# Performance work log

Measured on AMD Instinct MI355X. Metric: run time of the kernel, lower is better.

## Reference

```python
import jax, jax.numpy as jnp
import numpy as np

# Dims: B batch, L seq, D model dim, A attn dim, H heads, W window, FF ff hidden
B, L, D = 4, 4096, 1024
A, H, W = 64, 1, 64
FF = 2 * D
EPS = 1e-6


def setup_inputs() -> dict:
    key = jax.random.key(0)
    ks = jax.random.split(key, 12)
    s = lambda k, shape, scale: (jax.random.normal(k, shape, jnp.float32) * scale)
    return {
        "x": s(ks[0], (B, L, D), 1.0),
        "norm1_w": jnp.ones((D,), jnp.float32),
        "norm2_w": jnp.ones((D,), jnp.float32),
        "a_raw": s(ks[1], (D,), 1.0),   # diag SSM transition (pre-sigmoid)
        "b_w": s(ks[2], (D,), 0.5),     # diag input gain
        "c_w": s(ks[3], (D,), 0.5),     # diag output gain
        "Wq": s(ks[4], (D, A), D ** -0.5),
        "Wk": s(ks[5], (D, A), D ** -0.5),
        "Wv": s(ks[6], (D, A), D ** -0.5),
        "Wo": s(ks[7], (A, D), A ** -0.5),
        "Wg": s(ks[8], (D, 1), D ** -0.5),
        "gate_bias": jnp.float32(-4.0),
        "ff_w1": s(ks[9], (D, FF), D ** -0.5),
        "ff_w2": s(ks[10], (FF, D), FF ** -0.5),
    }


def rmsnorm(x, w):
    return x * jax.lax.rsqrt(jnp.mean(x * x, -1, keepdims=True) + EPS) * w


def ssm_scan(u, a):
    # h_t = a * h_{t-1} + u_t (diagonal linear recurrence), parallel assoc scan over time
    aa = jnp.broadcast_to(a, u.shape)

    def comb(c1, c2):
        a1, b1 = c1
        a2, b2 = c2
        return a1 * a2, a2 * b1 + b2

    _, h = jax.lax.associative_scan(comb, (aa, u), axis=1)
    return h


def reference(x, norm1_w, norm2_w, a_raw, b_w, c_w, Wq, Wk, Wv, Wo, Wg, gate_bias, ff_w1, ff_w2):
    normed = rmsnorm(x, norm1_w)                      # input_norm
    a = jax.nn.sigmoid(a_raw)                         # decay in (0,1)
    h = ssm_scan(normed * b_w, a)                     # ChaosSSMCore diag scan
    x_ssm = x + h * c_w                               # residual

    # Causal sliding-window attention sidecar (window W, includes self)
    K = x_ssm @ Wk                                    # [B,L,A]
    V = x_ssm @ Wv
    hd = A // H
    q = (x_ssm @ Wq).reshape(B, L, H, hd)
    idx = jnp.arange(L)[:, None] + jnp.arange(W)[None, :] - (W - 1)  # [L,W]
    valid = idx >= 0
    idxc = jnp.clip(idx, 0, L - 1)
    Kg = K[:, idxc].reshape(B, L, W, H, hd)           # gathered window keys
    Vg = V[:, idxc].reshape(B, L, W, H, hd)
    scores = jnp.einsum('blhd,blwhd->blhw', q, Kg) / jnp.sqrt(jnp.float32(hd))
    scores = jnp.where(valid[None, :, None, :], scores, -jnp.inf)
    p = jax.nn.softmax(scores, axis=-1)
    attn = jnp.einsum('blhw,blwhd->blhd', p, Vg).reshape(B, L, A) @ Wo

    gate = jax.nn.sigmoid(x_ssm @ Wg + gate_bias)     # near-zero gate at init
    x_ssm = x_ssm + gate * attn

    n2 = rmsnorm(x_ssm, norm2_w)                      # ff_norm
    y = x_ssm + jax.nn.silu(n2 @ ff_w1) @ ff_w2       # FeedForward residual
    return y
```

## Files before the change

### kernel.cpp

```cpp
#include <hip/hip_runtime.h>
#include <math.h>

#define B_ 4
#define L_ 4096
#define D_ 1024
#define A_ 64
#define FF_ 2048
#define N_ (B_*L_)
#define EPS_ 1e-6f
#define CHUNK_ 128
#define NCHUNK_ (L_/CHUNK_)

typedef __attribute__((ext_vector_type(8))) short bf16x8;
typedef __attribute__((ext_vector_type(4))) short s16x4;
typedef __attribute__((ext_vector_type(4))) float f32x4;

static __device__ __forceinline__ float sigmoidf_(float x) { return 1.f/(1.f+expf(-x)); }
static __device__ __forceinline__ float siluf_(float x)    { return x/(1.f+expf(-x)); }

static __device__ __forceinline__ unsigned short f2bf(float f) {
    unsigned u = __float_as_uint(f);
    u += 0x7fffu + ((u >> 16) & 1u);
    return (unsigned short)(u >> 16);
}

static __device__ __forceinline__ void gload16(const short* g, short* l) {
    __builtin_amdgcn_global_load_lds(
        (const __attribute__((address_space(1))) void*)g,
        (__attribute__((address_space(3))) void*)l, 16, 0, 0);
}

__global__ __launch_bounds__(256) void rms_kernel(const float* __restrict__ x,
                                                  float* __restrict__ rms)
{
    int row  = blockIdx.x*4 + (threadIdx.x>>6);
    int lane = threadIdx.x & 63;
    const float4* xr = (const float4*)(x + (size_t)row*D_);
    float s = 0.f;
#pragma unroll
    for (int j = 0; j < 4; j++) {
        float4 v = xr[lane + 64*j];
        s += v.x*v.x + v.y*v.y + v.z*v.z + v.w*v.w;
    }
#pragma unroll
    for (int off = 32; off > 0; off >>= 1) s += __shfl_xor(s, off);
    if (lane == 0) rms[row] = rsqrtf(s*(1.f/(float)D_) + EPS_);
}

__global__ __launch_bounds__(64) void scan1_kernel(
    const float* __restrict__ x, const float* __restrict__ rms1,
    const float* __restrict__ n1w, const float* __restrict__ bw,
    const float* __restrict__ araw, float* __restrict__ cpart)
{
    int d = blockIdx.x*64 + threadIdx.x;
    int c = blockIdx.y;
    int b = blockIdx.z;
    float a = sigmoidf_(araw[d]);
    float w = n1w[d]*bw[d];
    float h = 0.f;
    size_t base = ((size_t)b*L_ + (size_t)c*CHUNK_)*D_ + d;
    const float* rp = rms1 + b*L_ + c*CHUNK_;
#pragma unroll 8
    for (int t = 0; t < CHUNK_; t++) {
        float u = x[base + (size_t)t*D_] * rp[t] * w;
        h = a*h + u;
    }
    cpart[((size_t)b*NCHUNK_ + c)*D_ + d] = h;
}

__global__ __launch_bounds__(256) void scan2_kernel(
    const float* __restrict__ araw, const float* __restrict__ cpart,
    float* __restrict__ cin)
{
    int idx = blockIdx.x*256 + threadIdx.x;
    int b = idx >> 10;
    int d = idx & (D_-1);
    float a = sigmoidf_(araw[d]);
    float aT = a;
#pragma unroll
    for (int i = 0; i < 7; i++) aT *= aT;
    float cy = 0.f;
    for (int c = 0; c < NCHUNK_; c++) {
        size_t o = ((size_t)b*NCHUNK_ + c)*D_ + d;
        cin[o] = cy;
        cy = aT*cy + cpart[o];
    }
}

__global__ __launch_bounds__(64) void scan3_kernel(
    const float* __restrict__ x, const float* __restrict__ rms1,
    const float* __restrict__ n1w, const float* __restrict__ bw,
    const float* __restrict__ cw, const float* __restrict__ araw,
    const float* __restrict__ cin, float* __restrict__ x_ssm,
    short* __restrict__ xsb)
{
    int d = blockIdx.x*64 + threadIdx.x;
    int c = blockIdx.y;
    int b = blockIdx.z;
    float a = sigmoidf_(araw[d]);
    float w = n1w[d]*bw[d];
    float cwd = cw[d];
    float h = cin[((size_t)b*NCHUNK_ + c)*D_ + d];
    size_t base = ((size_t)b*L_ + (size_t)c*CHUNK_)*D_ + d;
    const float* rp = rms1 + b*L_ + c*CHUNK_;
#pragma unroll 8
    for (int t = 0; t < CHUNK_; t++) {
        size_t p = base + (size_t)t*D_;
        float xv = x[p];
        h = a*h + xv * rp[t] * w;
        float o = xv + h*cwd;
        x_ssm[p] = o;
        xsb[p] = (short)f2bf(o);
    }
}

__global__ __launch_bounds__(256) void gate_kernel(
    const float* __restrict__ xs, const float* __restrict__ Wg,
    const float* __restrict__ gb, float* __restrict__ gate)
{
    int row  = blockIdx.x*4 + (threadIdx.x>>6);
    int lane = threadIdx.x & 63;
    const float4* xr = (const float4*)(xs + (size_t)row*D_);
    const float4* wr = (const float4*)Wg;
    float s = 0.f;
#pragma unroll
    for (int j = 0; j < 4; j++) {
        float4 xv = xr[lane + 64*j];
        float4 wv = wr[lane + 64*j];
        s += xv.x*wv.x + xv.y*wv.y + xv.z*wv.z + xv.w*wv.w;
    }
#pragma unroll
    for (int off = 32; off > 0; off >>= 1) s += __shfl_xor(s, off);
    if (lane == 0) gate[row] = sigmoidf_(s + gb[0]);
}

__global__ __launch_bounds__(256) void attn_kernel(
    const float* __restrict__ qm, const float* __restrict__ km,
    const float* __restrict__ vm, short* __restrict__ om)
{
    __shared__ float KV[128][68];
    int b  = blockIdx.y;
    int l0 = blockIdx.x*64;
    int t  = threadIdx.x;
    int r  = t >> 2;
    int qq = t & 3;

#pragma unroll
    for (int i = 0; i < 8; i++) {
        int lin = i*256 + t;
        int row = lin >> 4;
        int f4  = lin & 15;
        int gl  = l0 - 64 + row;
        float4 val = make_float4(0.f,0.f,0.f,0.f);
        if (gl >= 0) val = *(const float4*)(km + ((size_t)b*L_ + gl)*A_ + f4*4);
        *(float4*)&KV[row][f4*4] = val;
    }
    float4 qreg[16];
    {
        const float* qrow = qm + ((size_t)b*L_ + l0 + r)*A_;
#pragma unroll
        for (int j = 0; j < 16; j++) qreg[j] = *(const float4*)(qrow + j*4);
    }
    __syncthreads();

    float s[16];
#pragma unroll
    for (int wi = 0; wi < 16; wi++) {
        int w  = qq*16 + wi;
        int tr = r + w + 1;
        float dot = 0.f;
#pragma unroll
        for (int j = 0; j < 16; j++) {
            float4 kv = *(const float4*)&KV[tr][j*4];
            dot += qreg[j].x*kv.x + qreg[j].y*kv.y + qreg[j].z*kv.z + qreg[j].w*kv.w;
        }
        s[wi] = (l0 + r - 63 + w >= 0) ? dot*0.125f : -INFINITY;
    }
    float mx = s[0];
#pragma unroll
    for (int wi = 1; wi < 16; wi++) mx = fmaxf(mx, s[wi]);
    mx = fmaxf(mx, __shfl_xor(mx, 1));
    mx = fmaxf(mx, __shfl_xor(mx, 2));
    float sum = 0.f;
#pragma unroll
    for (int wi = 0; wi < 16; wi++) { s[wi] = expf(s[wi] - mx); sum += s[wi]; }
    sum += __shfl_xor(sum, 1);
    sum += __shfl_xor(sum, 2);
    float inv = 1.f/sum;
#pragma unroll
    for (int wi = 0; wi < 16; wi++) s[wi] *= inv;

    __syncthreads();
#pragma unroll
    for (int i = 0; i < 8; i++) {
        int lin = i*256 + t;
        int row = lin >> 4;
        int f4  = lin & 15;
        int gl  = l0 - 64 + row;
        float4 val = make_float4(0.f,0.f,0.f,0.f);
        if (gl >= 0) val = *(const float4*)(vm + ((size_t)b*L_ + gl)*A_ + f4*4);
        *(float4*)&KV[row][f4*4] = val;
    }
    __syncthreads();

    float4 acc[4];
#pragma unroll
    for (int ss = 0; ss < 4; ss++) acc[ss] = make_float4(0.f,0.f,0.f,0.f);
#pragma unroll
    for (int w = 0; w < 64; w++) {
        float pv = __shfl(s[w & 15], (t & 60) + (w >> 4));
        int tr = r + w + 1;
#pragma unroll
        for (int ss = 0; ss < 4; ss++) {
            float4 vv = *(const float4*)&KV[tr][qq*16 + ss*4];
            acc[ss].x += pv*vv.x; acc[ss].y += pv*vv.y;
            acc[ss].z += pv*vv.z; acc[ss].w += pv*vv.w;
        }
    }
    short* orow = om + ((size_t)b*L_ + l0 + r)*A_ + qq*16;
#pragma unroll
    for (int ss = 0; ss < 4; ss++) {
        s16x4 ov = { (short)f2bf(acc[ss].x), (short)f2bf(acc[ss].y),
                     (short)f2bf(acc[ss].z), (short)f2bf(acc[ss].w) };
        *(s16x4*)(orow + ss*4) = ov;
    }
}

__global__ __launch_bounds__(256) void cvt_transpose(
    const float* __restrict__ in, int R, int C, short* __restrict__ out)
{
    __shared__ short sh[64][68];
    int t  = threadIdx.x;
    int c0 = blockIdx.x * 64, r0 = blockIdx.y * 64;
    int rr = t >> 4, cc = (t & 15) * 4;
#pragma unroll
    for (int p = 0; p < 4; p++) {
        int r = p*16 + rr;
        float4 v = *(const float4*)(in + (size_t)(r0 + r)*C + c0 + cc);
        s16x4 sv = { (short)f2bf(v.x), (short)f2bf(v.y), (short)f2bf(v.z), (short)f2bf(v.w) };
        *(s16x4*)&sh[r][cc] = sv;
    }
    __syncthreads();
#pragma unroll
    for (int p = 0; p < 4; p++) {
        int c = p*16 + rr;
        s16x4 ov = { sh[cc+0][c], sh[cc+1][c], sh[cc+2][c], sh[cc+3][c] };
        *(s16x4*)(out + (size_t)(c0 + c)*R + r0 + cc) = ov;
    }
}

__global__ __launch_bounds__(256) void ff1prep(
    const float* __restrict__ xatt, const float* __restrict__ n2w,
    short* __restrict__ a1)
{
    int row  = blockIdx.x*4 + (threadIdx.x>>6);
    int lane = threadIdx.x & 63;
    const float4* xr = (const float4*)(xatt + (size_t)row*D_);
    const float4* wr = (const float4*)n2w;
    float4 v[4];
    float s = 0.f;
#pragma unroll
    for (int j = 0; j < 4; j++) {
        v[j] = xr[lane + 64*j];
        s += v[j].x*v[j].x + v[j].y*v[j].y + v[j].z*v[j].z + v[j].w*v[j].w;
    }
#pragma unroll
    for (int off = 32; off > 0; off >>= 1) s += __shfl_xor(s, off);
    float r = rsqrtf(s*(1.f/(float)D_) + EPS_);
#pragma unroll
    for (int j = 0; j < 4; j++) {
        float4 w = wr[lane + 64*j];
        s16x4 o = { (short)f2bf(v[j].x*r*w.x), (short)f2bf(v[j].y*r*w.y),
                    (short)f2bf(v[j].z*r*w.z), (short)f2bf(v[j].w*r*w.w) };
        *(s16x4*)(a1 + (size_t)row*D_ + (lane + 64*j)*4) = o;
    }
}

__global__ __launch_bounds__(256) void qkv_mfma(
    const short* __restrict__ A, const short* __restrict__ BT,
    float* __restrict__ qo, float* __restrict__ ko, float* __restrict__ vo)
{
    __shared__ short As2[2][64*32];
    __shared__ short Bs2[2][192*32];
    const int t = threadIdx.x, l = t & 63, w = t >> 6;
    const size_t m0 = (size_t)blockIdx.x*64;
    const short* Ab = A + m0*D_;

    const int ar = w*16 + (l&15);
    const int offA = ar*32 + (((l>>4) ^ ((ar>>1)&3)) & 3)*8;
    int offB[12];
#pragma unroll
    for (int j = 0; j < 12; j++) {
        int br = j*16 + (l&15);
        offB[j] = br*32 + (((l>>4) ^ ((br>>1)&3)) & 3)*8;
    }

#define QSTG(bi, k0) { \
        { int r = t>>2; int lc = (t&3) ^ ((r>>1)&3); \
          gload16(Ab + (size_t)r*D_ + (k0) + lc*8, &As2[bi][(w*64)*8]); } \
        _Pragma("unroll") \
        for (int i_ = 0; i_ < 3; i_++) { \
            int s_ = i_*256 + t; int r = s_>>2; int lc = (s_&3) ^ ((r>>1)&3); \
            gload16(BT + (size_t)r*D_ + (k0) + lc*8, &Bs2[bi][(i_*256 + w*64)*8]); } }

    f32x4 acc[12];
    f32x4 zero = {0.f,0.f,0.f,0.f};
#pragma unroll
    for (int j = 0; j < 12; j++) acc[j] = zero;

    QSTG(0, 0);
    __syncthreads();
    int cur = 0;
    for (int kt = 0; kt < 32; kt++) {
        if (kt + 1 < 32) QSTG(cur^1, (kt+1)*32);
        bf16x8 af = *(const bf16x8*)&As2[cur][offA];
#pragma unroll
        for (int j = 0; j < 12; j++) {
            bf16x8 bfv = *(const bf16x8*)&Bs2[cur][offB[j]];
            acc[j] = __builtin_amdgcn_mfma_f32_16x16x32_bf16(af, bfv, acc[j], 0, 0, 0);
        }
        __syncthreads();
        cur ^= 1;
    }
#pragma unroll
    for (int j = 0; j < 12; j++) {
        int col = j*16 + (l&15);
        int mat = col >> 6, c = col & 63;
        float* dst = (mat == 0) ? qo : (mat == 1) ? ko : vo;
#pragma unroll
        for (int v = 0; v < 4; v++) {
            size_t row = m0 + w*16 + (l>>4)*4 + v;
            dst[row*A_ + c] = acc[j][v];
        }
    }
#undef QSTG
}

__global__ __launch_bounds__(256) void gemm_wo(
    const short* __restrict__ A,
    const short* __restrict__ BT,
    const float* __restrict__ gate, const float* __restrict__ resid,
    float* __restrict__ Cout)
{
    __shared__ short As3[128*64];
    __shared__ short Bs3[128*64];
    const int t = threadIdx.x, l = t & 63, w = t >> 6;
    const int wm = w >> 1, wn = w & 1;
    const size_t m0 = (size_t)blockIdx.x*128, n0 = (size_t)blockIdx.y*128;

#pragma unroll
    for (int i = 0; i < 4; i++) {
        int s = i*256 + t;
        int r = s >> 3, lc = (s&7) ^ (r&7);
        gload16(A  + (m0 + r)*64 + lc*8, &As3[(i*256 + w*64)*8]);
        gload16(BT + (n0 + r)*64 + lc*8, &Bs3[(i*256 + w*64)*8]);
    }
    __syncthreads();

    f32x4 acc[4][4];
    f32x4 zero = {0.f,0.f,0.f,0.f};
#pragma unroll
    for (int i = 0; i < 4; i++)
#pragma unroll
        for (int j = 0; j < 4; j++) acc[i][j] = zero;

#pragma unroll
    for (int kk = 0; kk < 2; kk++) {
        bf16x8 af[4], bfv[4];
#pragma unroll
        for (int i = 0; i < 4; i++) {
            int ar = wm*64 + i*16 + (l&15);
            int pch = (kk*4 + (l>>4)) ^ (ar&7);
            af[i] = *(const bf16x8*)&As3[ar*64 + pch*8];
        }
#pragma unroll
        for (int j = 0; j < 4; j++) {
            int br = wn*64 + j*16 + (l&15);
            int pch = (kk*4 + (l>>4)) ^ (br&7);
            bfv[j] = *(const bf16x8*)&Bs3[br*64 + pch*8];
        }
#pragma unroll
        for (int i = 0; i < 4; i++)
#pragma unroll
            for (int j = 0; j < 4; j++)
                acc[i][j] = __builtin_amdgcn_mfma_f32_16x16x32_bf16(af[i], bfv[j], acc[i][j], 0, 0, 0);
    }

#pragma unroll
    for (int i = 0; i < 4; i++) {
#pragma unroll
        for (int v = 0; v < 4; v++) {
            size_t row = m0 + wm*64 + i*16 + (l>>4)*4 + v;
            float g = gate[row];
#pragma unroll
            for (int j = 0; j < 4; j++) {
                size_t col = n0 + wn*64 + j*16 + (l&15);
                Cout[row*D_ + col] = resid[row*D_ + col] + g*acc[i][j][v];
            }
        }
    }
}

template<int K, int MODE>
__global__ __launch_bounds__(512, 2) void gemm256(
    const short* __restrict__ A,
    const short* __restrict__ BT,
    void* __restrict__ Cout, int ldc)
{
    __shared__ short As[4][256*32];
    __shared__ short Bs[4][256*32];

    const int gy = gridDim.y;
    const int nwg = gridDim.x * gy;
    const int o = blockIdx.y * gridDim.x + blockIdx.x;
    const int q = nwg >> 3;
    const int swz = (o & 7)*q + (o >> 3);
    const int bx = swz / gy, by = swz % gy;

    const int t = threadIdx.x;
    const int l = t & 63;
    const int w = t >> 6;
    const int wm = w >> 2;
    const int wn = w & 3;
    const size_t m0 = (size_t)bx * 256;
    const size_t n0 = (size_t)by * 256;
    const short* Ab = A  + m0 * (size_t)K;
    const short* Bb = BT + n0 * (size_t)K;
    const int s0 = w*64 + l;

    int offA[8], offB[4];
#pragma unroll
    for (int i = 0; i < 8; i++) {
        int ar = wm*128 + i*16 + (l&15);
        offA[i] = ar*32 + (((l>>4) ^ ((ar>>1)&3)) & 3)*8;
    }
#pragma unroll
    for (int j = 0; j < 4; j++) {
        int br = wn*64 + j*16 + (l&15);
        offB[j] = br*32 + (((l>>4) ^ ((br>>1)&3)) & 3)*8;
    }

#define STAGE_A(bi, k0) { _Pragma("unroll") \
    for (int i_ = 0; i_ < 2; i_++) { \
        int s_ = i_*512 + s0; int r_ = s_>>2; int lc_ = (s_&3) ^ ((r_>>1)&3); \
        gload16(Ab + (size_t)r_*K + (k0) + lc_*8, &As[bi][(i_*512 + w*64)*8]); } }
#define STAGE_B(bi, k0) { _Pragma("unroll") \
    for (int i_ = 0; i_ < 2; i_++) { \
        int s_ = i_*512 + s0; int r_ = s_>>2; int lc_ = (s_&3) ^ ((r_>>1)&3); \
        gload16(Bb + (size_t)r_*K + (k0) + lc_*8, &Bs[bi][(i_*512 + w*64)*8]); } }

    f32x4 acc[8][4];
    f32x4 zero = {0.f,0.f,0.f,0.f};
#pragma unroll
    for (int i = 0; i < 8; i++)
#pragma unroll
        for (int j = 0; j < 4; j++) acc[i][j] = zero;

    STAGE_A(0, 0);  STAGE_B(0, 0);
    STAGE_A(1, 32); STAGE_B(1, 32);
    asm volatile("s_waitcnt vmcnt(4)" ::: "memory");
    __builtin_amdgcn_s_barrier();

    const int nk = K >> 5;
#pragma unroll 1
    for (int kt = 0; kt < nk; kt++) {
        const short* a_ = &As[kt & 3][0];
        const short* b_ = &Bs[kt & 3][0];
        const int prefetch = (kt + 2 < nk);
        const int pb = (kt + 2) & 3;
        const int pk = (kt + 2) << 5;

        bf16x8 bfv[4], af[4];
#pragma unroll
        for (int j = 0; j < 4; j++) bfv[j] = *(const bf16x8*)(b_ + offB[j]);
#pragma unroll
        for (int i = 0; i < 4; i++) af[i] = *(const bf16x8*)(a_ + offA[i]);
        if (prefetch) STAGE_A(pb, pk);
        __builtin_amdgcn_s_setprio(1);
#pragma unroll
        for (int i = 0; i < 4; i++)
#pragma unroll
            for (int j = 0; j < 4; j++)
                acc[i][j] = __builtin_amdgcn_mfma_f32_16x16x32_bf16(af[i], bfv[j], acc[i][j], 0, 0, 0);
        __builtin_amdgcn_s_setprio(0);

#pragma unroll
        for (int i = 0; i < 4; i++) af[i] = *(const bf16x8*)(a_ + offA[4+i]);
        if (prefetch) STAGE_B(pb, pk);
        __builtin_amdgcn_s_setprio(1);
#pragma unroll
        for (int i = 0; i < 4; i++)
#pragma unroll
            for (int j = 0; j < 4; j++)
                acc[4+i][j] = __builtin_amdgcn_mfma_f32_16x16x32_bf16(af[i], bfv[j], acc[4+i][j], 0, 0, 0);
        __builtin_amdgcn_s_setprio(0);

        if (prefetch) { asm volatile("s_waitcnt vmcnt(4)" ::: "memory"); }
        else          { asm volatile("s_waitcnt vmcnt(0)" ::: "memory"); }
        __builtin_amdgcn_s_barrier();
    }

#pragma unroll
    for (int i = 0; i < 8; i++) {
        size_t row_base = m0 + wm*128 + i*16 + (l >> 4)*4;
#pragma unroll
        for (int j = 0; j < 4; j++) {
            size_t col = n0 + wn*64 + j*16 + (l & 15);
#pragma unroll
            for (int v = 0; v < 4; v++) {
                size_t row = row_base + v;
                float val = acc[i][j][v];
                if (MODE == 0) {
                    ((short*)Cout)[row * ldc + col] = (short)f2bf(siluf_(val));
                } else {
                    float* p = (float*)Cout + row * ldc + col;
                    *p = val + *p;
                }
            }
        }
    }
#undef STAGE_A
#undef STAGE_B
}

extern "C" void kernel_launch(void* const* d_in, const int* in_sizes, int n_in,
                              void* d_out, int out_size, void* d_ws, size_t ws_size,
                              hipStream_t stream)
{
    const float* x    = (const float*)d_in[0];
    const float* n1w  = (const float*)d_in[1];
    const float* n2w  = (const float*)d_in[2];
    const float* araw = (const float*)d_in[3];
    const float* bw   = (const float*)d_in[4];
    const float* cw   = (const float*)d_in[5];
    const float* Wq   = (const float*)d_in[6];
    const float* Wk   = (const float*)d_in[7];
    const float* Wv   = (const float*)d_in[8];
    const float* Wo   = (const float*)d_in[9];
    const float* Wg   = (const float*)d_in[10];
    const float* gb   = (const float*)d_in[11];
    const float* ffw1 = (const float*)d_in[12];
    const float* ffw2 = (const float*)d_in[13];
    float* out = (float*)d_out;

    float* ws    = (float*)d_ws;
    float* rms1  = ws;
    float* gate  = rms1  + N_;
    float* cpart = gate  + N_;
    float* cin   = cpart + (size_t)B_*NCHUNK_*D_;
    float* qb    = cin   + (size_t)B_*NCHUNK_*D_;
    float* kb    = qb    + (size_t)N_*A_;
    float* vb    = kb    + (size_t)N_*A_;
    float* x_ssm = vb    + (size_t)N_*A_;
    short* xsb   = (short*)(x_ssm + (size_t)N_*D_);
    short* attnb = xsb   + (size_t)N_*D_;
    short* a1    = attnb + (size_t)N_*A_;
    short* act   = a1    + (size_t)N_*D_;
    short* w1t   = act   + (size_t)N_*FF_;
    short* w2t   = w1t   + (size_t)FF_*D_;
    short* wqkvT = w2t   + (size_t)D_*FF_;
    short* wot   = wqkvT + (size_t)192*D_;

    cvt_transpose<<<dim3(FF_/64, D_/64), 256, 0, stream>>>(ffw1, D_, FF_, w1t);
    cvt_transpose<<<dim3(D_/64, FF_/64), 256, 0, stream>>>(ffw2, FF_, D_, w2t);
    cvt_transpose<<<dim3(1, D_/64), 256, 0, stream>>>(Wq, D_, A_, wqkvT);
    cvt_transpose<<<dim3(1, D_/64), 256, 0, stream>>>(Wk, D_, A_, wqkvT + (size_t)A_*D_);
    cvt_transpose<<<dim3(1, D_/64), 256, 0, stream>>>(Wv, D_, A_, wqkvT + (size_t)2*A_*D_);
    cvt_transpose<<<dim3(D_/64, 1), 256, 0, stream>>>(Wo, A_, D_, wot);

    rms_kernel<<<N_/4, 256, 0, stream>>>(x, rms1);
    scan1_kernel<<<dim3(D_/64, NCHUNK_, B_), 64, 0, stream>>>(x, rms1, n1w, bw, araw, cpart);
    scan2_kernel<<<(B_*D_)/256, 256, 0, stream>>>(araw, cpart, cin);
    scan3_kernel<<<dim3(D_/64, NCHUNK_, B_), 64, 0, stream>>>(x, rms1, n1w, bw, cw, araw, cin, x_ssm, xsb);
    qkv_mfma<<<N_/64, 256, 0, stream>>>(xsb, wqkvT, qb, kb, vb);
    gate_kernel<<<N_/4, 256, 0, stream>>>(x_ssm, Wg, gb, gate);
    attn_kernel<<<dim3(L_/64, B_), 256, 0, stream>>>(qb, kb, vb, attnb);
    gemm_wo<<<dim3(N_/128, D_/128), 256, 0, stream>>>(attnb, wot, gate, x_ssm, out);
    ff1prep<<<N_/4, 256, 0, stream>>>(out, n2w, a1);
    gemm256<D_, 0><<<dim3(N_/256, FF_/256), 512, 0, stream>>>(a1, w1t, (void*)act, FF_);
    gemm256<FF_, 1><<<dim3(N_/256, D_/256), 512, 0, stream>>>(act, w2t, (void*)out, D_);
}
```

Before: 478.2 us.

## Rewrite FFN GEMMs as 8-phase ping-pong pipeline and merge QKV weight transposes

The FFN GEMM kernel is restructured to use K-tiles of 64, double-buffered half-tiles of A and B in a single 128KB LDS array with XOR swizzle, and four MFMA phases per iteration. Each phase is separated by barriers that interleave global-to-LDS prefetch of the next tile with compute, in the style of the public 8-wave ping-pong schedule. The warp-to-tile mapping also changes to a 2x4 interleaved layout. Separately, the three Q/K/V weight transposes are merged into one launch. The deeper schedule adds more barriers and uses LDS that could limit occupancy to 2 blocks per CU.

Result: slower. 494.6 us (+3.4%).

```diff
diff --git a/kernel.cpp b/kernel.cpp
--- a/kernel.cpp
+++ b/kernel.cpp
@@ -249,6 +249,32 @@
     }
 }
 
+__global__ __launch_bounds__(256) void qkv_t3(
+    const float* __restrict__ Wq, const float* __restrict__ Wk,
+    const float* __restrict__ Wv, short* __restrict__ outall)
+{
+    __shared__ short sh[64][68];
+    const float* in = (blockIdx.z == 0) ? Wq : (blockIdx.z == 1) ? Wk : Wv;
+    short* out = outall + (size_t)blockIdx.z * A_ * D_;
+    int t  = threadIdx.x;
+    int r0 = blockIdx.y * 64;
+    int rr = t >> 4, cc = (t & 15) * 4;
+#pragma unroll
+    for (int p = 0; p < 4; p++) {
+        int r = p*16 + rr;
+        float4 v = *(const float4*)(in + (size_t)(r0 + r)*A_ + cc);
+        s16x4 sv = { (short)f2bf(v.x), (short)f2bf(v.y), (short)f2bf(v.z), (short)f2bf(v.w) };
+        *(s16x4*)&sh[r][cc] = sv;
+    }
+    __syncthreads();
+#pragma unroll
+    for (int p = 0; p < 4; p++) {
+        int c = p*16 + rr;
+        s16x4 ov = { sh[cc+0][c], sh[cc+1][c], sh[cc+2][c], sh[cc+3][c] };
+        *(s16x4*)(out + (size_t)c*D_ + r0 + cc) = ov;
+    }
+}
+
 __global__ __launch_bounds__(256) void ff1prep(
     const float* __restrict__ xatt, const float* __restrict__ n2w,
     short* __restrict__ a1)
@@ -402,52 +428,55 @@
 }
 
 template<int K, int MODE>
-__global__ __launch_bounds__(512, 2) void gemm256(
+__global__ __launch_bounds__(512, 2) void gemm8p(
     const short* __restrict__ A,
     const short* __restrict__ BT,
     void* __restrict__ Cout, int ldc)
 {
-    __shared__ short As[4][256*32];
-    __shared__ short Bs[4][256*32];
-
-    const int gy = gridDim.y;
-    const int nwg = gridDim.x * gy;
-    const int o = blockIdx.y * gridDim.x + blockIdx.x;
+    __shared__ short LDSb[65536];
+
+    const int gx = gridDim.x, gy = gridDim.y;
+    const int nwg = gx*gy;
+    const int o = blockIdx.y*gx + blockIdx.x;
     const int q = nwg >> 3;
     const int swz = (o & 7)*q + (o >> 3);
     const int bx = swz / gy, by = swz % gy;
 
-    const int t = threadIdx.x;
-    const int l = t & 63;
-    const int w = t >> 6;
-    const int wm = w >> 2;
-    const int wn = w & 3;
-    const size_t m0 = (size_t)bx * 256;
-    const size_t n0 = (size_t)by * 256;
-    const short* Ab = A  + m0 * (size_t)K;
-    const short* Bb = BT + n0 * (size_t)K;
-    const int s0 = w*64 + l;
-
-    int offA[8], offB[4];
-#pragma unroll
-    for (int i = 0; i < 8; i++) {
-        int ar = wm*128 + i*16 + (l&15);
-        offA[i] = ar*32 + (((l>>4) ^ ((ar>>1)&3)) & 3)*8;
-    }
-#pragma unroll
-    for (int j = 0; j < 4; j++) {
-        int br = wn*64 + j*16 + (l&15);
-        offB[j] = br*32 + (((l>>4) ^ ((br>>1)&3)) & 3)*8;
-    }
-
-#define STAGE_A(bi, k0) { _Pragma("unroll") \
-    for (int i_ = 0; i_ < 2; i_++) { \
-        int s_ = i_*512 + s0; int r_ = s_>>2; int lc_ = (s_&3) ^ ((r_>>1)&3); \
-        gload16(Ab + (size_t)r_*K + (k0) + lc_*8, &As[bi][(i_*512 + w*64)*8]); } }
-#define STAGE_B(bi, k0) { _Pragma("unroll") \
-    for (int i_ = 0; i_ < 2; i_++) { \
-        int s_ = i_*512 + s0; int r_ = s_>>2; int lc_ = (s_&3) ^ ((r_>>1)&3); \
-        gload16(Bb + (size_t)r_*K + (k0) + lc_*8, &Bs[bi][(i_*512 + w*64)*8]); } }
+    const int t = threadIdx.x, l = t & 63, w = t >> 6;
+    const int wm = w & 1;
+    const int wn = w >> 1;
+    const size_t m0 = (size_t)bx*256, n0 = (size_t)by*256;
+    const short* Ab = A  + m0*(size_t)K;
+    const short* Bb = BT + n0*(size_t)K;
+
+    const int l15 = l & 15;
+    const int l16 = (l >> 4)*16;
+    const int xsw = (l & 7)*16;
+    const int sc_row = l >> 3;
+    const int sc_gc  = ((l&7) ^ sc_row)*8;
+
+#define ASLOT(db,h) (((db)*2 + (h))*8192)
+#define BSLOT(db,h) (32768 + ((db)*2 + (h))*8192)
+
+    auto stage = [&](const short* src, int baseSlot, int h, int ktile) {
+#pragma unroll
+        for (int ii = 0; ii < 2; ii++) {
+            int chunk = ii*8 + w;
+            gload16(src + (size_t)(h*128 + chunk*8 + sc_row)*K + ktile*64 + sc_gc,
+                    (short*)&LDSb[baseSlot + chunk*512]);
+        }
+    };
+    auto rdA = [&](int db, int h, int ip, int kk) {
+        int rl = ip*32 + wm*16 + l15;
+        int cb = (kk*64 + l16) ^ xsw;
+        return *(const bf16x8*)&LDSb[ASLOT(db,h) + rl*64 + (cb>>1)];
+    };
+    auto rdB = [&](int db, int jj, int kk) {
+        int h = jj >> 1;
+        int rl = (jj&1)*64 + wn*16 + l15;
+        int cb = (kk*64 + l16) ^ xsw;
+        return *(const bf16x8*)&LDSb[BSLOT(db,h) + rl*64 + (cb>>1)];
+    };
 
     f32x4 acc[8][4];
     f32x4 zero = {0.f,0.f,0.f,0.f};
@@ -456,56 +485,116 @@
 #pragma unroll
         for (int j = 0; j < 4; j++) acc[i][j] = zero;
 
-    STAGE_A(0, 0);  STAGE_B(0, 0);
-    STAGE_A(1, 32); STAGE_B(1, 32);
-    asm volatile("s_waitcnt vmcnt(4)" ::: "memory");
+    const int nk = K >> 6;
+    bf16x8 ar[4][2], br[4][2];
+
+    stage(Ab, ASLOT(0,0), 0, 0);
+    stage(Bb, BSLOT(0,0), 0, 0);
+    stage(Ab, ASLOT(0,1), 1, 0);
+    stage(Bb, BSLOT(0,1), 1, 0);
+    stage(Ab, ASLOT(1,0), 0, 1);
+    stage(Bb, BSLOT(1,0), 0, 1);
+    asm volatile("s_waitcnt vmcnt(8)" ::: "memory");
     __builtin_amdgcn_s_barrier();
 
-    const int nk = K >> 5;
 #pragma unroll 1
     for (int kt = 0; kt < nk; kt++) {
-        const short* a_ = &As[kt & 3][0];
-        const short* b_ = &Bs[kt & 3][0];
-        const int prefetch = (kt + 2 < nk);
-        const int pb = (kt + 2) & 3;
-        const int pk = (kt + 2) << 5;
-
-        bf16x8 bfv[4], af[4];
-#pragma unroll
-        for (int j = 0; j < 4; j++) bfv[j] = *(const bf16x8*)(b_ + offB[j]);
-#pragma unroll
-        for (int i = 0; i < 4; i++) af[i] = *(const bf16x8*)(a_ + offA[i]);
-        if (prefetch) STAGE_A(pb, pk);
+        const int db = kt & 1, dn = (kt+1) & 1;
+        const bool s1 = (kt+1 < nk), s2 = (kt+2 < nk);
+
+#pragma unroll
+        for (int i2 = 0; i2 < 4; i2++)
+#pragma unroll
+            for (int kk = 0; kk < 2; kk++) ar[i2][kk] = rdA(db, 0, i2, kk);
+#pragma unroll
+        for (int jj = 0; jj < 2; jj++)
+#pragma unroll
+            for (int kk = 0; kk < 2; kk++) br[jj][kk] = rdB(db, jj, kk);
+        if (s1) stage(Ab, ASLOT(dn,1), 1, kt+1);
+        if (s1) { asm volatile("s_waitcnt vmcnt(6)" ::: "memory"); }
+        else    { asm volatile("s_waitcnt vmcnt(0)" ::: "memory"); }
+        __builtin_amdgcn_s_barrier();
+        asm volatile("s_waitcnt lgkmcnt(0)" ::: "memory");
+        __builtin_amdgcn_sched_barrier(0);
         __builtin_amdgcn_s_setprio(1);
 #pragma unroll
-        for (int i = 0; i < 4; i++)
-#pragma unroll
-            for (int j = 0; j < 4; j++)
-                acc[i][j] = __builtin_amdgcn_mfma_f32_16x16x32_bf16(af[i], bfv[j], acc[i][j], 0, 0, 0);
+        for (int i2 = 0; i2 < 4; i2++)
+#pragma unroll
+            for (int jj = 0; jj < 2; jj++)
+#pragma unroll
+                for (int kk = 0; kk < 2; kk++)
+                    acc[i2][jj] = __builtin_amdgcn_mfma_f32_16x16x32_bf16(
+                        ar[i2][kk], br[jj][kk], acc[i2][jj], 0, 0, 0);
         __builtin_amdgcn_s_setprio(0);
-
-#pragma unroll
-        for (int i = 0; i < 4; i++) af[i] = *(const bf16x8*)(a_ + offA[4+i]);
-        if (prefetch) STAGE_B(pb, pk);
+        __builtin_amdgcn_s_barrier();
+
+#pragma unroll
+        for (int jj = 0; jj < 2; jj++)
+#pragma unroll
+            for (int kk = 0; kk < 2; kk++) br[2+jj][kk] = rdB(db, 2+jj, kk);
+        if (s1) stage(Bb, BSLOT(dn,1), 1, kt+1);
+        if (s1) { asm volatile("s_waitcnt vmcnt(8)" ::: "memory"); }
+        else    { asm volatile("s_waitcnt vmcnt(0)" ::: "memory"); }
+        __builtin_amdgcn_s_barrier();
+        asm volatile("s_waitcnt lgkmcnt(0)" ::: "memory");
+        __builtin_amdgcn_sched_barrier(0);
         __builtin_amdgcn_s_setprio(1);
 #pragma unroll
-        for (int i = 0; i < 4; i++)
-#pragma unroll
-            for (int j = 0; j < 4; j++)
-                acc[4+i][j] = __builtin_amdgcn_mfma_f32_16x16x32_bf16(af[i], bfv[j], acc[4+i][j], 0, 0, 0);
+        for (int i2 = 0; i2 < 4; i2++)
+#pragma unroll
+            for (int jj = 0; jj < 2; jj++)
+#pragma unroll
+                for (int kk = 0; kk < 2; kk++)
+                    acc[i2][2+jj] = __builtin_amdgcn_mfma_f32_16x16x32_bf16(
+                        ar[i2][kk], br[2+jj][kk], acc[i2][2+jj], 0, 0, 0);
         __builtin_amdgcn_s_setprio(0);
-
-        if (prefetch) { asm volatile("s_waitcnt vmcnt(4)" ::: "memory"); }
-        else          { asm volatile("s_waitcnt vmcnt(0)" ::: "memory"); }
+        __builtin_amdgcn_s_barrier();
+
+#pragma unroll
+        for (int i2 = 0; i2 < 4; i2++)
+#pragma unroll
+            for (int kk = 0; kk < 2; kk++) ar[i2][kk] = rdA(db, 1, i2, kk);
+        if (s2) stage(Ab, ASLOT(db,0), 0, kt+2);
+        __builtin_amdgcn_s_barrier();
+        asm volatile("s_waitcnt lgkmcnt(0)" ::: "memory");
+        __builtin_amdgcn_sched_barrier(0);
+        __builtin_amdgcn_s_setprio(1);
+#pragma unroll
+        for (int i2 = 0; i2 < 4; i2++)
+#pragma unroll
+            for (int jj = 0; jj < 2; jj++)
+#pragma unroll
+                for (int kk = 0; kk < 2; kk++)
+                    acc[4+i2][jj] = __builtin_amdgcn_mfma_f32_16x16x32_bf16(
+                        ar[i2][kk], br[jj][kk], acc[4+i2][jj], 0, 0, 0);
+        __builtin_amdgcn_s_setprio(0);
+        __builtin_amdgcn_s_barrier();
+
+        if (s2) stage(Bb, BSLOT(db,0), 0, kt+2);
+        if (s2)      { asm volatile("s_waitcnt vmcnt(8)" ::: "memory"); }
+        else if (s1) { asm volatile("s_waitcnt vmcnt(4)" ::: "memory"); }
+        else         { asm volatile("s_waitcnt vmcnt(0)" ::: "memory"); }
+        __builtin_amdgcn_s_barrier();
+        __builtin_amdgcn_sched_barrier(0);
+        __builtin_amdgcn_s_setprio(1);
+#pragma unroll
+        for (int i2 = 0; i2 < 4; i2++)
+#pragma unroll
+            for (int jj = 0; jj < 2; jj++)
+#pragma unroll
+                for (int kk = 0; kk < 2; kk++)
+                    acc[4+i2][2+jj] = __builtin_amdgcn_mfma_f32_16x16x32_bf16(
+                        ar[i2][kk], br[2+jj][kk], acc[4+i2][2+jj], 0, 0, 0);
+        __builtin_amdgcn_s_setprio(0);
         __builtin_amdgcn_s_barrier();
     }
 
 #pragma unroll
     for (int i = 0; i < 8; i++) {
-        size_t row_base = m0 + wm*128 + i*16 + (l >> 4)*4;
+        size_t row_base = m0 + (size_t)(i>>2)*128 + (i&3)*32 + wm*16 + (l>>4)*4;
 #pragma unroll
         for (int j = 0; j < 4; j++) {
-            size_t col = n0 + wn*64 + j*16 + (l & 15);
+            size_t col = n0 + (size_t)j*64 + wn*16 + l15;
 #pragma unroll
             for (int v = 0; v < 4; v++) {
                 size_t row = row_base + v;
@@ -519,8 +608,8 @@
             }
         }
     }
-#undef STAGE_A
-#undef STAGE_B
+#undef ASLOT
+#undef BSLOT
 }
 
 extern "C" void kernel_launch(void* const* d_in, const int* in_sizes, int n_in,
@@ -563,9 +652,7 @@
 
     cvt_transpose<<<dim3(FF_/64, D_/64), 256, 0, stream>>>(ffw1, D_, FF_, w1t);
     cvt_transpose<<<dim3(D_/64, FF_/64), 256, 0, stream>>>(ffw2, FF_, D_, w2t);
-    cvt_transpose<<<dim3(1, D_/64), 256, 0, stream>>>(Wq, D_, A_, wqkvT);
-    cvt_transpose<<<dim3(1, D_/64), 256, 0, stream>>>(Wk, D_, A_, wqkvT + (size_t)A_*D_);
-    cvt_transpose<<<dim3(1, D_/64), 256, 0, stream>>>(Wv, D_, A_, wqkvT + (size_t)2*A_*D_);
+    qkv_t3<<<dim3(1, D_/64, 3), 256, 0, stream>>>(Wq, Wk, Wv, wqkvT);
     cvt_transpose<<<dim3(D_/64, 1), 256, 0, stream>>>(Wo, A_, D_, wot);
 
     rms_kernel<<<N_/4, 256, 0, stream>>>(x, rms1);
@@ -577,6 +664,6 @@
     attn_kernel<<<dim3(L_/64, B_), 256, 0, stream>>>(qb, kb, vb, attnb);
     gemm_wo<<<dim3(N_/128, D_/128), 256, 0, stream>>>(attnb, wot, gate, x_ssm, out);
     ff1prep<<<N_/4, 256, 0, stream>>>(out, n2w, a1);
-    gemm256<D_, 0><<<dim3(N_/256, FF_/256), 512, 0, stream>>>(a1, w1t, (void*)act, FF_);
-    gemm256<FF_, 1><<<dim3(N_/256, D_/256), 512, 0, stream>>>(act, w2t, (void*)out, D_);
-}
+    gemm8p<D_, 0><<<dim3(N_/256, FF_/256), 512, 0, stream>>>(a1, w1t, (void*)act, FF_);
+    gemm8p<FF_, 1><<<dim3(N_/256, D_/256), 512, 0, stream>>>(act, w2t, (void*)out, D_);
+}
```
